# Optimization experiments

Hardware: AMD Instinct MI355X
Metric: run time of the kernel (lower is better)

Reference implementation:

```python
import jax, jax.numpy as jnp
import numpy as np

A = -0.75  # PyTorch bicubic convolution constant

def _cubic_weights(t):
    # t: fractional part in [0,1). Returns the 4 tap weights
    # (matches PyTorch get_cubic_upsample_coefficients with A=-0.75).
    t1 = t + 1.0
    w0 = ((A * t1 - 5.0 * A) * t1 + 8.0 * A) * t1 - 4.0 * A
    w1 = ((A + 2.0) * t - (A + 3.0)) * t * t + 1.0
    s = 1.0 - t
    w2 = ((A + 2.0) * s - (A + 3.0)) * s * s + 1.0
    s2 = 2.0 - t
    w3 = ((A * s2 - 5.0 * A) * s2 + 8.0 * A) * s2 - 4.0 * A
    return (w0, w1, w2, w3)

def _reflect_index(i, size):
    # integer reflection for padding_mode='reflection', align_corners=True over [0, size-1]
    span = size - 1
    if span <= 0:
        return jnp.zeros_like(i)
    m = jnp.abs(i) % (2 * span)
    return jnp.where(m > span, 2 * span - m, m)

def _bicubic_warp(x, flow):
    # x: [B,C,H,W], flow: [B,2,H,W] (flow[:,0]=dx, flow[:,1]=dy)
    B, C, H, W = x.shape
    gx = jnp.arange(W, dtype=x.dtype)
    gy = jnp.arange(H, dtype=x.dtype)
    # normalize-to-[-1,1] then grid_sample unnormalize (align_corners=True) cancel exactly:
    ix = gx[None, None, :] + flow[:, 0]  # [B,H,W] source x coord
    iy = gy[None, :, None] + flow[:, 1]  # [B,H,W] source y coord
    bx = jnp.floor(ix)
    by = jnp.floor(iy)
    tx = ix - bx
    ty = iy - by
    bx = bx.astype(jnp.int32)
    by = by.astype(jnp.int32)
    wx = _cubic_weights(tx)
    wy = _cubic_weights(ty)
    xf = x.reshape(B, C, H * W)
    out = jnp.zeros_like(x)
    for j in range(4):  # fixed 4x4 tap stencil
        Y = _reflect_index(by + (j - 1), H)
        for i in range(4):
            X = _reflect_index(bx + (i - 1), W)
            idx = (Y * W + X).reshape(B, 1, H * W)
            v = jnp.take_along_axis(xf, idx, axis=2).reshape(B, C, H, W)
            out = out + v * (wy[j] * wx[i])[:, None]
    return out

def setup_inputs() -> dict:
    key = jax.random.key(0)
    k1, k2, k3 = jax.random.split(key, 3)
    B, C, H, W = 8, 4, 1024, 1024
    return {
        "input": jax.random.normal(k1, (B, C, H, W), dtype=jnp.float32),
        "target": jax.random.normal(k2, (B, C, H, W), dtype=jnp.float32),
        "flow": jax.random.normal(k3, (B, 2, H, W), dtype=jnp.float32),
    }

def reference(input, target, flow):
    warped = _bicubic_warp(target, flow)
    b = 5
    return jnp.mean(jnp.abs(input[..., b:-b, b:-b] - warped[..., b:-b, b:-b]))
```

## Files before the change

kernel.cpp:

```cpp
#include <hip/hip_runtime.h>

constexpr int BB = 8, CC = 4, HH = 1024, WW = 1024, CROP = 5;
constexpr int HC = HH - 2 * CROP, WC = WW - 2 * CROP;
constexpr int HW = HH * WW;
constexpr float AA = -0.75f;

constexpr int NSTRIP = 16;
constexpr int GRID = 32 * NSTRIP;
constexpr int RING = 16;
constexpr int SWID = 272;
constexpr int CH_STRIDE = RING * SWID;

typedef __attribute__((address_space(1))) const void gv_t;
typedef __attribute__((address_space(3))) void lv_t;

__device__ __forceinline__ int reflect_small(int i) {
    int r = i < 0 ? -i : i;
    return r > (HH - 1) ? 2 * (HH - 1) - r : r;
}

__device__ __forceinline__ void cubic_w(float t, float& w0, float& w1,
                                        float& w2, float& w3) {
    float t1 = t + 1.0f;
    w0 = ((AA * t1 - 5.0f * AA) * t1 + 8.0f * AA) * t1 - 4.0f * AA;
    w1 = ((AA + 2.0f) * t - (AA + 3.0f)) * t * t + 1.0f;
    float s = 1.0f - t;
    w2 = ((AA + 2.0f) * s - (AA + 3.0f)) * s * s + 1.0f;
    float s2 = 2.0f - t;
    w3 = ((AA * s2 - 5.0f * AA) * s2 + 8.0f * AA) * s2 - 4.0f * AA;
}

__device__ __noinline__ float px_slow(const float* __restrict__ tgt_b,
                                      const float* __restrict__ in_b, int pix,
                                      int bx, int by, float wx0, float wx1,
                                      float wx2, float wx3, float wy0,
                                      float wy1, float wy2, float wy3) {
    const int r0 = reflect_small(by - 1) * WW;
    const int r1 = reflect_small(by) * WW;
    const int r2 = reflect_small(by + 1) * WW;
    const int r3 = reflect_small(by + 2) * WW;
    const int c0 = reflect_small(bx - 1);
    const int c1 = reflect_small(bx);
    const int c2 = reflect_small(bx + 1);
    const int c3 = reflect_small(bx + 2);
    float acc = 0.0f;
#pragma unroll
    for (int c = 0; c < CC; ++c) {
        const float* tb = tgt_b + c * HW;
        float q0 = wx0 * tb[r0 + c0] + wx1 * tb[r0 + c1] + wx2 * tb[r0 + c2] +
                   wx3 * tb[r0 + c3];
        float q1 = wx0 * tb[r1 + c0] + wx1 * tb[r1 + c1] + wx2 * tb[r1 + c2] +
                   wx3 * tb[r1 + c3];
        float q2 = wx0 * tb[r2 + c0] + wx1 * tb[r2 + c1] + wx2 * tb[r2 + c2] +
                   wx3 * tb[r2 + c3];
        float q3 = wx0 * tb[r3 + c0] + wx1 * tb[r3 + c1] + wx2 * tb[r3 + c2] +
                   wx3 * tb[r3 + c3];
        float v = wy0 * q0 + wy1 * q1 + wy2 * q2 + wy3 * q3;
        acc += fabsf(in_b[c * HW + pix] - v);
    }
    return acc;
}

__global__ __launch_bounds__(256, 2) void warp_loss_k(
    const float* __restrict__ input, const float* __restrict__ target,
    const float* __restrict__ flow, float* __restrict__ wsbuf) {
    __shared__ float cache[CC * CH_STRIDE];
    const int tid = (int)threadIdx.x;
    const int wv = tid >> 6, lane = tid & 63;

    const int colid = (int)blockIdx.x & 31;
    const int strip = (int)blockIdx.x >> 5;
    const int b = colid >> 2;
    const int chunk = colid & 3;
    const int x0 = CROP + chunk * 256;
    const int wscol = chunk == 0 ? 0 : chunk == 1 ? 252 : chunk == 2 ? 508 : 752;
    const int y0 = CROP + strip * 64;
    const int y1 = min(y0 + 64, CROP + HC);

    const int x = x0 + tid;
    const bool valid_px = x <= 1018;
    const int xc = valid_px ? x : 1018;

    const float* tgt_b = target + (size_t)b * CC * HW;
    const float* in_b = input + (size_t)b * CC * HW;
    const float* flow_b = flow + (size_t)b * 2 * HW;

    const float* plane = tgt_b + (size_t)wv * HW;
    const int chbase = wv * CH_STRIDE;

#pragma unroll 1
    for (int k = 0; k < 11; ++k) {
        const int r = y0 - 5 + k;
        const int slot = r & (RING - 1);
        const float* src = plane + (size_t)r * WW + wscol;
        __builtin_amdgcn_global_load_lds((gv_t*)(src + lane * 4),
                                         (lv_t*)&cache[chbase + slot * SWID],
                                         16, 0, 0);
        __builtin_amdgcn_global_load_lds(
            (gv_t*)(src + 208 + lane),
            (lv_t*)&cache[chbase + slot * SWID + 208], 4, 0, 0);
    }
    __syncthreads();

    float lsum = 0.0f;

    for (int y = y0; y < y1; ++y) {
        {
            const int r = y + 6;
            if (r < HH) {
                const int slot = r & (RING - 1);
                const float* src = plane + (size_t)r * WW + wscol;
                __builtin_amdgcn_global_load_lds(
                    (gv_t*)(src + lane * 4),
                    (lv_t*)&cache[chbase + slot * SWID], 16, 0, 0);
                __builtin_amdgcn_global_load_lds(
                    (gv_t*)(src + 208 + lane),
                    (lv_t*)&cache[chbase + slot * SWID + 208], 4, 0, 0);
            }
        }

        const int pix = y * WW + xc;
        const float dx = flow_b[pix];
        const float dy = flow_b[HW + pix];
        const float i0v = in_b[pix];
        const float i1v = in_b[HW + pix];
        const float i2v = in_b[2 * HW + pix];
        const float i3v = in_b[3 * HW + pix];

        const float fx = (float)xc + dx;
        const float fy = (float)y + dy;
        const float bxf = floorf(fx), byf = floorf(fy);
        const int bx = (int)bxf, by = (int)byf;
        const float tx = fx - bxf, ty = fy - byf;

        float wx0, wx1, wx2, wx3, wy0, wy1, wy2, wy3;
        cubic_w(tx, wx0, wx1, wx2, wx3);
        cubic_w(ty, wy0, wy1, wy2, wy3);

        const int d = by - y;
        const int cx = bx - 1 - wscol;
        const bool fast =
            valid_px & (d >= -4) & (d <= 3) & (cx >= 0) & (cx <= 268);

        if (fast) {
            const int t = (by - 1) & (RING - 1);
            float v0 = 0.0f, v1 = 0.0f, v2 = 0.0f, v3 = 0.0f;
#pragma unroll
            for (int j = 0; j < 4; ++j) {
                const int s = (t + j) & (RING - 1);
                const int base = s * SWID + cx;
                const float wyj =
                    j == 0 ? wy0 : j == 1 ? wy1 : j == 2 ? wy2 : wy3;
                const float* p0 = &cache[base];
                const float* p1 = &cache[CH_STRIDE + base];
                const float* p2 = &cache[2 * CH_STRIDE + base];
                const float* p3 = &cache[3 * CH_STRIDE + base];
                v0 += wyj * (p0[0] * wx0 + p0[1] * wx1 + p0[2] * wx2 + p0[3] * wx3);
                v1 += wyj * (p1[0] * wx0 + p1[1] * wx1 + p1[2] * wx2 + p1[3] * wx3);
                v2 += wyj * (p2[0] * wx0 + p2[1] * wx1 + p2[2] * wx2 + p2[3] * wx3);
                v3 += wyj * (p3[0] * wx0 + p3[1] * wx1 + p3[2] * wx2 + p3[3] * wx3);
            }
            lsum += fabsf(i0v - v0) + fabsf(i1v - v1) + fabsf(i2v - v2) +
                    fabsf(i3v - v3);
        } else if (valid_px) {
            lsum += px_slow(tgt_b, in_b, pix, bx, by, wx0, wx1, wx2, wx3,
                            wy0, wy1, wy2, wy3);
        }

        __syncthreads();
    }

#pragma unroll
    for (int off2 = 32; off2 > 0; off2 >>= 1) lsum += __shfl_down(lsum, off2);

    __shared__ float sm[4];
    if (lane == 0) sm[wv] = lsum;
    __syncthreads();
    if (tid == 0) wsbuf[blockIdx.x] = sm[0] + sm[1] + sm[2] + sm[3];
}

__global__ __launch_bounds__(1024) void reduce_k(const float* __restrict__ ws,
                                                 float* __restrict__ out) {
    float s = 0.0f;
    for (int i = threadIdx.x; i < GRID; i += 1024) s += ws[i];
#pragma unroll
    for (int off = 32; off > 0; off >>= 1) s += __shfl_down(s, off);
    __shared__ float sm[16];
    const int lane = threadIdx.x & 63;
    const int wv = threadIdx.x >> 6;
    if (lane == 0) sm[wv] = s;
    __syncthreads();
    if (threadIdx.x == 0) {
        float t = 0.0f;
#pragma unroll
        for (int i = 0; i < 16; ++i) t += sm[i];
        constexpr float inv_count = 1.0f / ((float)BB * CC * HC * WC);
        out[0] = t * inv_count;
    }
}

extern "C" void kernel_launch(void* const* d_in, const int* in_sizes, int n_in,
                              void* d_out, int out_size, void* d_ws,
                              size_t ws_size, hipStream_t stream) {
    const float* input = (const float*)d_in[0];
    const float* target = (const float*)d_in[1];
    const float* flow = (const float*)d_in[2];
    float* ws = (float*)d_ws;
    float* out = (float*)d_out;

    warp_loss_k<<<GRID, 256, 0, stream>>>(input, target, flow, ws);
    reduce_k<<<1, 1024, 0, stream>>>(ws, out);
}
```

Before: 130.2 us.

## Split channels into pairs across blocks to halve LDS and raise occupancy

Each block now handles only two of the four channels, which doubles the grid and halves the LDS ring cache per block, and launch bounds are raised to 4 blocks per SIMD-group. Two waves now share each channel's row load, one doing the vector part and one the tail. The aim is higher occupancy to hide gather and load latency. The cost is that flow loads and the cubic weight math are repeated in both channel-pair blocks, and flow traffic doubles.

```diff
diff --git a/kernel.cpp b/kernel.cpp
--- a/kernel.cpp
+++ b/kernel.cpp
@@ -6,7 +6,7 @@
 constexpr float AA = -0.75f;
 
 constexpr int NSTRIP = 16;
-constexpr int GRID = 32 * NSTRIP;
+constexpr int GRID = 32 * NSTRIP * 2;
 constexpr int RING = 16;
 constexpr int SWID = 272;
 constexpr int CH_STRIDE = RING * SWID;
@@ -30,11 +30,11 @@
     w3 = ((AA * s2 - 5.0f * AA) * s2 + 8.0f * AA) * s2 - 4.0f * AA;
 }
 
-__device__ __noinline__ float px_slow(const float* __restrict__ tgt_b,
-                                      const float* __restrict__ in_b, int pix,
-                                      int bx, int by, float wx0, float wx1,
-                                      float wx2, float wx3, float wy0,
-                                      float wy1, float wy2, float wy3) {
+__device__ __noinline__ float px_slow2(const float* __restrict__ tgt_p,
+                                       const float* __restrict__ in_p, int pix,
+                                       int bx, int by, float wx0, float wx1,
+                                       float wx2, float wx3, float wy0,
+                                       float wy1, float wy2, float wy3) {
     const int r0 = reflect_small(by - 1) * WW;
     const int r1 = reflect_small(by) * WW;
     const int r2 = reflect_small(by + 1) * WW;
@@ -45,8 +45,8 @@
     const int c3 = reflect_small(bx + 2);
     float acc = 0.0f;
 #pragma unroll
-    for (int c = 0; c < CC; ++c) {
-        const float* tb = tgt_b + c * HW;
+    for (int c = 0; c < 2; ++c) {
+        const float* tb = tgt_p + c * HW;
         float q0 = wx0 * tb[r0 + c0] + wx1 * tb[r0 + c1] + wx2 * tb[r0 + c2] +
                    wx3 * tb[r0 + c3];
         float q1 = wx0 * tb[r1 + c0] + wx1 * tb[r1 + c1] + wx2 * tb[r1 + c2] +
@@ -56,20 +56,22 @@
         float q3 = wx0 * tb[r3 + c0] + wx1 * tb[r3 + c1] + wx2 * tb[r3 + c2] +
                    wx3 * tb[r3 + c3];
         float v = wy0 * q0 + wy1 * q1 + wy2 * q2 + wy3 * q3;
-        acc += fabsf(in_b[c * HW + pix] - v);
+        acc += fabsf(in_p[c * HW + pix] - v);
     }
     return acc;
 }
 
-__global__ __launch_bounds__(256, 2) void warp_loss_k(
+__global__ __launch_bounds__(256, 4) void warp_loss_k(
     const float* __restrict__ input, const float* __restrict__ target,
     const float* __restrict__ flow, float* __restrict__ wsbuf) {
-    __shared__ float cache[CC * CH_STRIDE];
+    __shared__ float cache[2 * CH_STRIDE];
     const int tid = (int)threadIdx.x;
     const int wv = tid >> 6, lane = tid & 63;
 
-    const int colid = (int)blockIdx.x & 31;
-    const int strip = (int)blockIdx.x >> 5;
+    const int low = (int)blockIdx.x & 511;
+    const int pair = (int)blockIdx.x >> 9;
+    const int colid = low >> 4;
+    const int strip = low & 15;
     const int b = colid >> 2;
     const int chunk = colid & 3;
     const int x0 = CROP + chunk * 256;
@@ -81,24 +83,28 @@
     const bool valid_px = x <= 1018;
     const int xc = valid_px ? x : 1018;
 
-    const float* tgt_b = target + (size_t)b * CC * HW;
-    const float* in_b = input + (size_t)b * CC * HW;
+    const float* tgt_p = target + (size_t)b * CC * HW + (size_t)(pair * 2) * HW;
+    const float* in_p = input + (size_t)b * CC * HW + (size_t)(pair * 2) * HW;
     const float* flow_b = flow + (size_t)b * 2 * HW;
 
-    const float* plane = tgt_b + (size_t)wv * HW;
-    const int chbase = wv * CH_STRIDE;
+    const int chv = wv >> 1, part = wv & 1;
+    const float* plane = tgt_p + (size_t)chv * HW;
+    const int chbase = chv * CH_STRIDE;
 
 #pragma unroll 1
     for (int k = 0; k < 11; ++k) {
         const int r = y0 - 5 + k;
         const int slot = r & (RING - 1);
         const float* src = plane + (size_t)r * WW + wscol;
-        __builtin_amdgcn_global_load_lds((gv_t*)(src + lane * 4),
-                                         (lv_t*)&cache[chbase + slot * SWID],
-                                         16, 0, 0);
-        __builtin_amdgcn_global_load_lds(
-            (gv_t*)(src + 208 + lane),
-            (lv_t*)&cache[chbase + slot * SWID + 208], 4, 0, 0);
+        if (part == 0) {
+            __builtin_amdgcn_global_load_lds(
+                (gv_t*)(src + lane * 4), (lv_t*)&cache[chbase + slot * SWID],
+                16, 0, 0);
+        } else {
+            __builtin_amdgcn_global_load_lds(
+                (gv_t*)(src + 208 + lane),
+                (lv_t*)&cache[chbase + slot * SWID + 208], 4, 0, 0);
+        }
     }
     __syncthreads();
 
@@ -110,22 +116,23 @@
             if (r < HH) {
                 const int slot = r & (RING - 1);
                 const float* src = plane + (size_t)r * WW + wscol;
-                __builtin_amdgcn_global_load_lds(
-                    (gv_t*)(src + lane * 4),
-                    (lv_t*)&cache[chbase + slot * SWID], 16, 0, 0);
-                __builtin_amdgcn_global_load_lds(
-                    (gv_t*)(src + 208 + lane),
-                    (lv_t*)&cache[chbase + slot * SWID + 208], 4, 0, 0);
+                if (part == 0) {
+                    __builtin_amdgcn_global_load_lds(
+                        (gv_t*)(src + lane * 4),
+                        (lv_t*)&cache[chbase + slot * SWID], 16, 0, 0);
+                } else {
+                    __builtin_amdgcn_global_load_lds(
+                        (gv_t*)(src + 208 + lane),
+                        (lv_t*)&cache[chbase + slot * SWID + 208], 4, 0, 0);
+                }
             }
         }
 
         const int pix = y * WW + xc;
         const float dx = flow_b[pix];
         const float dy = flow_b[HW + pix];
-        const float i0v = in_b[pix];
-        const float i1v = in_b[HW + pix];
-        const float i2v = in_b[2 * HW + pix];
-        const float i3v = in_b[3 * HW + pix];
+        const float i0v = in_p[pix];
+        const float i1v = in_p[HW + pix];
 
         const float fx = (float)xc + dx;
         const float fy = (float)y + dy;
@@ -144,7 +151,7 @@
 
         if (fast) {
             const int t = (by - 1) & (RING - 1);
-            float v0 = 0.0f, v1 = 0.0f, v2 = 0.0f, v3 = 0.0f;
+            float v0 = 0.0f, v1 = 0.0f;
 #pragma unroll
             for (int j = 0; j < 4; ++j) {
                 const int s = (t + j) & (RING - 1);
@@ -153,18 +160,13 @@
                     j == 0 ? wy0 : j == 1 ? wy1 : j == 2 ? wy2 : wy3;
                 const float* p0 = &cache[base];
                 const float* p1 = &cache[CH_STRIDE + base];
-                const float* p2 = &cache[2 * CH_STRIDE + base];
-                const float* p3 = &cache[3 * CH_STRIDE + base];
                 v0 += wyj * (p0[0] * wx0 + p0[1] * wx1 + p0[2] * wx2 + p0[3] * wx3);
                 v1 += wyj * (p1[0] * wx0 + p1[1] * wx1 + p1[2] * wx2 + p1[3] * wx3);
-                v2 += wyj * (p2[0] * wx0 + p2[1] * wx1 + p2[2] * wx2 + p2[3] * wx3);
-                v3 += wyj * (p3[0] * wx0 + p3[1] * wx1 + p3[2] * wx2 + p3[3] * wx3);
             }
-            lsum += fabsf(i0v - v0) + fabsf(i1v - v1) + fabsf(i2v - v2) +
-                    fabsf(i3v - v3);
+            lsum += fabsf(i0v - v0) + fabsf(i1v - v1);
         } else if (valid_px) {
-            lsum += px_slow(tgt_b, in_b, pix, bx, by, wx0, wx1, wx2, wx3,
-                            wy0, wy1, wy2, wy3);
+            lsum += px_slow2(tgt_p, in_p, pix, bx, by, wx0, wx1, wx2, wx3,
+                             wy0, wy1, wy2, wy3);
         }
 
         __syncthreads();
```

Result: no change. 129.8 us (-0.3%).
